# Kernel optimization log

Measured on AMD Instinct MI355X. Metric: run time of the kernel, lower is better.

Reference implementation:

```python
import jax, jax.numpy as jnp
import numpy as np


def _cell(xt, h, c, Wih, Whh, b):
    # Single LSTM cell step; PyTorch gate order i, f, g, o.
    g = xt @ Wih.T + h @ Whh.T + b
    i, f, gg, o = jnp.split(g, 4, axis=-1)
    c = jax.nn.sigmoid(f) * c + jax.nn.sigmoid(i) * jnp.tanh(gg)
    h = jax.nn.sigmoid(o) * jnp.tanh(c)
    return h, c


def _lstm_layer(x, Wih, Whh, b):
    # x: [B, T, D] -> hs: [B, T, H], (h, c): final states [B, H]
    B = x.shape[0]
    H = Whh.shape[1]
    h0 = jnp.zeros((B, H), x.dtype)
    c0 = jnp.zeros((B, H), x.dtype)

    def step(carry, xt):
        h, c = carry
        h, c = _cell(xt, h, c, Wih, Whh, b)
        return (h, c), h

    (h, c), hs = jax.lax.scan(step, (h0, c0), jnp.swapaxes(x, 0, 1))
    return jnp.swapaxes(hs, 0, 1), h, c


def setup_inputs() -> dict:
    key = jax.random.key(0)
    B, T_SRC, D_IN, H, TGT = 512, 256, 32, 128, 64
    ks = iter(jax.random.split(key, 32))
    s_in = 1.0 / np.sqrt(H)

    def u(k, shape):
        return jax.random.uniform(k, shape, jnp.float32, -s_in, s_in)

    inp = {"x": jax.random.normal(next(ks), (B, T_SRC, D_IN), jnp.float32),
           "target_len": TGT}
    for pre in ("enc", "dec"):
        for l, din in ((0, D_IN), (1, H)):
            inp[f"{pre}_Wih{l}"] = u(next(ks), (4 * H, din))
            inp[f"{pre}_Whh{l}"] = u(next(ks), (4 * H, H))
            inp[f"{pre}_bih{l}"] = u(next(ks), (4 * H,))
            inp[f"{pre}_bhh{l}"] = u(next(ks), (4 * H,))
    inp["lin_W"] = u(next(ks), (D_IN, H))
    inp["lin_b"] = u(next(ks), (D_IN,))
    return inp


def reference(x, target_len,
              enc_Wih0, enc_Whh0, enc_bih0, enc_bhh0,
              enc_Wih1, enc_Whh1, enc_bih1, enc_bhh1,
              dec_Wih0, dec_Whh0, dec_bih0, dec_bhh0,
              dec_Wih1, dec_Whh1, dec_bih1, dec_bhh1,
              lin_W, lin_b):
    # --- encoder: 2-layer full-sequence LSTM, zero initial state ---
    hs0, eh0, ec0 = _lstm_layer(x, enc_Wih0, enc_Whh0, enc_bih0 + enc_bhh0)
    _, eh1, ec1 = _lstm_layer(hs0, enc_Wih1, enc_Whh1, enc_bih1 + enc_bhh1)

    # --- decoder: recursive single-step LSTM + linear head, fed back ---
    db0 = dec_bih0 + dec_bhh0
    db1 = dec_bih1 + dec_bhh1
    dec_in0 = x[:, -1, :]  # last source step

    def step(carry, _):
        h0, c0, h1, c1, inp = carry
        h0, c0 = _cell(inp, h0, c0, dec_Wih0, dec_Whh0, db0)
        h1, c1 = _cell(h0, h1, c1, dec_Wih1, dec_Whh1, db1)
        out = h1 @ lin_W.T + lin_b
        return (h0, c0, h1, c1, out), out

    _, outs = jax.lax.scan(step, (eh0, ec0, eh1, ec1, dec_in0), None,
                           length=target_len)
    return jnp.swapaxes(outs, 0, 1)  # [B, target_len, input_size]
```

## Files before the change

### kernel.cpp

```cpp
#include <hip/hip_runtime.h>
#include <cstdint>
#include <cstddef>

typedef short  short8  __attribute__((ext_vector_type(8)));
typedef float  float4v __attribute__((ext_vector_type(4)));

#define MFMA_B16(a,b,c) __builtin_amdgcn_mfma_f32_16x16x32_bf16(a,b,c,0,0,0)

static constexpr int B_  = 512;
static constexpr int T_  = 256;
static constexpr int DIN = 32;
static constexpr int H_  = 128;
static constexpr int TGT = 64;

static constexpr float L2E  = 1.4426950408889634f;
static constexpr float L2E2 = 2.8853900817779268f;

static constexpr size_t OFF_XFRAG = 0;
static constexpr size_t OFF_EW0   = 8388608;
static constexpr size_t OFF_EW1LO = OFF_EW0   + 163840;
static constexpr size_t OFF_EW1HI = OFF_EW1LO + 131072;
static constexpr size_t OFF_DW0   = OFF_EW1HI + 131072;
static constexpr size_t OFF_DW1LO = OFF_DW0   + 163840;
static constexpr size_t OFF_DW1HI = OFF_DW1LO + 131072;
static constexpr size_t OFF_LIN   = OFF_DW1HI + 131072;
static constexpr size_t OFF_BIAS  = OFF_LIN   + 8192;
static constexpr size_t WS_NEED   = OFF_BIAS  + 8320;

static constexpr int SM_W    = 0;
static constexpr int SM_ABUF = 131072;
static constexpr int SM_INP  = 147712;
static constexpr int SM_LIN  = 148992;
static constexpr int SM_TOTAL= 157184;

__device__ __forceinline__ short f2bf(float f){
  unsigned u = __float_as_uint(f);
  unsigned r = (u + 0x7fffu + ((u>>16)&1u)) >> 16;
  return (short)(r & 0xffffu);
}
__device__ __forceinline__ float sigm2(float x){
  return __builtin_amdgcn_rcpf(1.f + __builtin_amdgcn_exp2f(-x));
}
__device__ __forceinline__ float st2(float a, float b){
  float ea = __builtin_amdgcn_exp2f(-a);
  float eb = __builtin_amdgcn_exp2f(-b);
  float d  = __builtin_amdgcn_rcpf((1.f+ea)*(1.f+eb));
  return (1.f-eb)*d;
}
__device__ __forceinline__ float st2c(float a, float c){
  float ea = __builtin_amdgcn_exp2f(-a);
  float eb = __builtin_amdgcn_exp2f(-L2E2*c);
  float d  = __builtin_amdgcn_rcpf((1.f+ea)*(1.f+eb));
  return (1.f-eb)*d;
}
__device__ __forceinline__ float gate_scale(int n){
  return ((n >> 7) == 2) ? L2E2 : L2E;
}

__global__ void prep_x_kernel(const float* __restrict__ x, short8* __restrict__ xfrag){
  int i = blockIdx.x*256 + threadIdx.x;
  if (i >= 32*256*64) return;
  int l    = i & 63;
  int t    = (i >> 6) & 255;
  int bblk = i >> 14;
  int b    = bblk*16 + (l & 15);
  const float* src = x + ((size_t)(b*T_ + t))*DIN + ((l>>4)*8);
  short8 v;
  #pragma unroll
  for (int j=0;j<8;j++) v[j] = f2bf(src[j]);
  xfrag[i] = v;
}

__device__ __forceinline__ void pack160(short8* __restrict__ dst,
                                        const float* __restrict__ Wih,
                                        const float* __restrict__ Whh,
                                        int e){
  int nt = e/320; int r = e%320; int kb = r/64; int l = r%64;
  int n  = nt*16 + (l&15);
  float s = gate_scale(n);
  short8 v;
  #pragma unroll
  for (int j=0;j<8;j++){
    int k = kb*32 + (l>>4)*8 + j;
    float f = (k < 32) ? Wih[n*32 + k] : Whh[n*128 + (k-32)];
    v[j] = f2bf(f*s);
  }
  dst[e] = v;
}
__device__ __forceinline__ void pack256s(short8* __restrict__ dlo, short8* __restrict__ dhi,
                                         const float* __restrict__ Wih,
                                         const float* __restrict__ Whh,
                                         int e){
  int nt = e/512; int r = e%512; int kb = r/64; int l = r%64;
  int n  = nt*16 + (l&15);
  float s = gate_scale(n);
  short8 v;
  #pragma unroll
  for (int j=0;j<8;j++){
    int k = kb*32 + (l>>4)*8 + j;
    float f = (k < 128) ? Wih[n*128 + k] : Whh[n*128 + (k-128)];
    v[j] = f2bf(f*s);
  }
  if (kb < 4) dlo[(nt*4 + kb)*64 + l]     = v;
  else        dhi[(nt*4 + (kb-4))*64 + l] = v;
}

__global__ void prep_w_kernel(
    const float* __restrict__ eWih0, const float* __restrict__ eWhh0,
    const float* __restrict__ eWih1, const float* __restrict__ eWhh1,
    const float* __restrict__ dWih0, const float* __restrict__ dWhh0,
    const float* __restrict__ dWih1, const float* __restrict__ dWhh1,
    const float* __restrict__ linW,
    const float* __restrict__ eb0a, const float* __restrict__ eb0b,
    const float* __restrict__ eb1a, const float* __restrict__ eb1b,
    const float* __restrict__ db0a, const float* __restrict__ db0b,
    const float* __restrict__ db1a, const float* __restrict__ db1b,
    const float* __restrict__ linb,
    short8* __restrict__ encW0,
    short8* __restrict__ encW1lo, short8* __restrict__ encW1hi,
    short8* __restrict__ decW0,
    short8* __restrict__ decW1lo, short8* __restrict__ decW1hi,
    short8* __restrict__ linT,  float* __restrict__ biases)
{
  int i = blockIdx.x*256 + threadIdx.x;
  if (i < 10240)       { pack160(encW0, eWih0, eWhh0, i); }
  else if (i < 26624)  { pack256s(encW1lo, encW1hi, eWih1, eWhh1, i-10240); }
  else if (i < 36864)  { pack160(decW0, dWih0, dWhh0, i-26624); }
  else if (i < 53248)  { pack256s(decW1lo, decW1hi, dWih1, dWhh1, i-36864); }
  else if (i < 53760)  {
    int e = i - 53248;
    int nt = e/256; int r = e%256; int kb = r/64; int l = r%64;
    int n = nt*16 + (l&15);
    short8 v;
    #pragma unroll
    for (int j=0;j<8;j++){
      int k = kb*32 + (l>>4)*8 + j;
      v[j] = f2bf(linW[n*128 + k]);
    }
    linT[e] = v;
  }
  else if (i < 55840)  {
    int e = i - 53760;
    float v;
    if      (e < 512)  v = (eb0a[e]       + eb0b[e]      ) * gate_scale(e);
    else if (e < 1024) v = (eb1a[e-512]   + eb1b[e-512]  ) * gate_scale(e-512);
    else if (e < 1536) v = (db0a[e-1024]  + db0b[e-1024] ) * gate_scale(e-1024);
    else if (e < 2048) v = (db1a[e-1536]  + db1b[e-1536] ) * gate_scale(e-1536);
    else               v = linb[e-2048];
    biases[e] = v;
  }
}

__global__ __launch_bounds__(512, 1) void lstm_main_kernel(
    const short8* __restrict__ xfrag,
    const short8* __restrict__ encW0,
    const short8* __restrict__ encW1lo, const short8* __restrict__ encW1hi,
    const short8* __restrict__ decW0,
    const short8* __restrict__ decW1lo, const short8* __restrict__ decW1hi,
    const short8* __restrict__ linT,  const float* __restrict__ biases,
    float* __restrict__ out)
{
  extern __shared__ __align__(16) char smem[];
  short8* Wlds        = (short8*)(smem + SM_W);
  short (*Abuf)[520]  = (short(*)[520])(smem + SM_ABUF);
  short (*inpA)[40]   = (short(*)[40])(smem + SM_INP);
  short8* Wlin        = (short8*)(smem + SM_LIN);

  const int tid  = threadIdx.x;
  const int w    = tid >> 6;
  const int l    = tid & 63;
  const int col  = l & 15;
  const int lq   = l >> 4;
  const int bblk = blockIdx.x;

  for (int i = tid; i < 8192; i += 512) Wlds[i] = encW1hi[i];
  for (int i = tid; i < 16*520; i += 512) ((short*)Abuf)[i] = 0;

  short8 W0r[4][5];
  short8 W1lo[4][4];
  #pragma unroll
  for (int i=0;i<4;i++){
    #pragma unroll
    for (int kb=0;kb<5;kb++) W0r[i][kb]  = encW0  [(size_t)(8*i+w)*320 + (size_t)kb*64 + l];
    #pragma unroll
    for (int kb=0;kb<4;kb++) W1lo[i][kb] = encW1lo[(size_t)(8*i+w)*256 + (size_t)kb*64 + l];
  }
  float bs0[4], bs1[4];
  #pragma unroll
  for (int i=0;i<4;i++){
    bs0[i] = biases[       (8*i+w)*16 + col];
    bs1[i] = biases[512 +  (8*i+w)*16 + col];
  }

  float c0[4] = {0.f,0.f,0.f,0.f};
  float c1[4] = {0.f,0.f,0.f,0.f};

  const short8* xf = xfrag + (size_t)bblk*T_*64 + l;
  short8 a0 = xf[0];
  __syncthreads();


  {
    short8 hp[4];
    #pragma unroll
    for (int kb=0;kb<4;kb++) hp[kb] = *(const short8*)&Abuf[col][128 + kb*32 + lq*8];
    float4v acc0[4];
    #pragma unroll
    for (int i4=0;i4<4;i4++){
      float4v a = {bs0[i4],bs0[i4],bs0[i4],bs0[i4]};
      a = MFMA_B16(a0, W0r[i4][0], a);
      #pragma unroll
      for (int kb=0;kb<4;kb++) a = MFMA_B16(hp[kb], W0r[i4][kb+1], a);
      acc0[i4] = a;
    }
    a0 = xf[64];
    #pragma unroll
    for (int q=0;q<4;q++){
      float cc = st2(acc0[0][q], acc0[2][q]);
      c0[q] = cc;
      Abuf[lq*4+q][0 + 16*w + col] = f2bf(st2c(acc0[3][q], cc));
    }
    __syncthreads();
  }

  #pragma unroll 2
  for (int i = 1; i < T_; i++){
    const int p_h0_r = ((i-1)&1)*128;
    const int p_h0_w = (i&1)*128;
    const int p_h1_r = 256 + (i&1)*128;
    const int p_h1_w = 256 + ((i-1)&1)*128;

    short8 hp[4], h1p[4];
    #pragma unroll
    for (int kb=0;kb<4;kb++) hp[kb]  = *(const short8*)&Abuf[col][p_h0_r + kb*32 + lq*8];
    #pragma unroll
    for (int kb=0;kb<4;kb++) h1p[kb] = *(const short8*)&Abuf[col][p_h1_r + kb*32 + lq*8];

    float4v acc0[4], acc1[4];
    #pragma unroll
    for (int i4=0;i4<4;i4++){
      float4v a = {bs0[i4],bs0[i4],bs0[i4],bs0[i4]};
      a = MFMA_B16(a0, W0r[i4][0], a);
      #pragma unroll
      for (int kb=0;kb<4;kb++) a = MFMA_B16(hp[kb], W0r[i4][kb+1], a);
      acc0[i4] = a;

      float4v b = {bs1[i4],bs1[i4],bs1[i4],bs1[i4]};
      #pragma unroll
      for (int kb=0;kb<4;kb++) b = MFMA_B16(hp[kb], W1lo[i4][kb], b);
      #pragma unroll
      for (int kb=0;kb<4;kb++){
        short8 wv = Wlds[((8*i4+w)*4 + kb)*64 + l];
        b = MFMA_B16(h1p[kb], wv, b);
      }
      acc1[i4] = b;
    }
    a0 = xf[(size_t)((i+1 < T_) ? i+1 : i)*64];

    #pragma unroll
    for (int q=0;q<4;q++){
      float cc = sigm2(acc0[1][q])*c0[q] + st2(acc0[0][q], acc0[2][q]);
      c0[q] = cc;
      Abuf[lq*4+q][p_h0_w + 16*w + col] = f2bf(st2c(acc0[3][q], cc));
    }
    #pragma unroll
    for (int q=0;q<4;q++){
      float cc = sigm2(acc1[1][q])*c1[q] + st2(acc1[0][q], acc1[2][q]);
      c1[q] = cc;
      Abuf[lq*4+q][p_h1_w + 16*w + col] = f2bf(st2c(acc1[3][q], cc));
    }
    __syncthreads();
  }

  {
    const int p_h0_r = 128;
    const int p_h1_r = 256 + 0;
    const int p_h1_w = 256 + 128;
    short8 hp[4], h1p[4];
    #pragma unroll
    for (int kb=0;kb<4;kb++) hp[kb]  = *(const short8*)&Abuf[col][p_h0_r + kb*32 + lq*8];
    #pragma unroll
    for (int kb=0;kb<4;kb++) h1p[kb] = *(const short8*)&Abuf[col][p_h1_r + kb*32 + lq*8];
    float4v acc1[4];
    #pragma unroll
    for (int i4=0;i4<4;i4++){
      float4v b = {bs1[i4],bs1[i4],bs1[i4],bs1[i4]};
      #pragma unroll
      for (int kb=0;kb<4;kb++) b = MFMA_B16(hp[kb], W1lo[i4][kb], b);
      #pragma unroll
      for (int kb=0;kb<4;kb++){
        short8 wv = Wlds[((8*i4+w)*4 + kb)*64 + l];
        b = MFMA_B16(h1p[kb], wv, b);
      }
      acc1[i4] = b;
    }
    #pragma unroll
    for (int q=0;q<4;q++){
      float cc = sigm2(acc1[1][q])*c1[q] + st2(acc1[0][q], acc1[2][q]);
      c1[q] = cc;
      Abuf[lq*4+q][p_h1_w + 16*w + col] = f2bf(st2c(acc1[3][q], cc));
    }
    __syncthreads();
  }

  for (int i = tid; i < 8192; i += 512) Wlds[i] = decW1hi[i];
  if (tid < 512) Wlin[tid] = linT[tid];
  #pragma unroll
  for (int i=0;i<4;i++){
    #pragma unroll
    for (int kb=0;kb<5;kb++) W0r[i][kb]  = decW0  [(size_t)(8*i+w)*320 + (size_t)kb*64 + l];
    #pragma unroll
    for (int kb=0;kb<4;kb++) W1lo[i][kb] = decW1lo[(size_t)(8*i+w)*256 + (size_t)kb*64 + l];
    bs0[i] = biases[1024 + (8*i+w)*16 + col];
    bs1[i] = biases[1536 + (8*i+w)*16 + col];
  }
  float blin = (w < 2) ? biases[2048 + w*16 + col] : 0.f;
  if (w == 0){
    *(short8*)&inpA[col][lq*8] = xf[(size_t)(T_-1)*64];
  }
  __syncthreads();

  #pragma unroll 2
  for (int td = 0; td < TGT; td++){
    const int h0r = ((td+1)&1) * 128;
    const int h0w = 128 - h0r;
    const int h1r = 256 + h0r;
    const int h1w = 256 + h0w;

    short8 a0d = *(const short8*)&inpA[col][lq*8];
    short8 ah[4];
    #pragma unroll
    for (int kb=0;kb<4;kb++) ah[kb] = *(const short8*)&Abuf[col][h0r + kb*32 + lq*8];
    float4v acc0[4];
    #pragma unroll
    for (int i=0;i<4;i++){
      float4v a = {bs0[i],bs0[i],bs0[i],bs0[i]};
      a = MFMA_B16(a0d, W0r[i][0], a);
      #pragma unroll
      for (int kb=0;kb<4;kb++) a = MFMA_B16(ah[kb], W0r[i][kb+1], a);
      acc0[i] = a;
    }
    #pragma unroll
    for (int q=0;q<4;q++){
      float cc = sigm2(acc0[1][q])*c0[q] + st2(acc0[0][q], acc0[2][q]);
      c0[q] = cc;
      Abuf[lq*4+q][h0w + 16*w + col] = f2bf(st2c(acc0[3][q], cc));
    }
    __syncthreads();

    short8 a1lo[4], a1hi[4];
    #pragma unroll
    for (int kb=0;kb<4;kb++) a1lo[kb] = *(const short8*)&Abuf[col][h0w + kb*32 + lq*8];
    #pragma unroll
    for (int kb=0;kb<4;kb++) a1hi[kb] = *(const short8*)&Abuf[col][h1r + kb*32 + lq*8];
    float4v acc1[4];
    #pragma unroll
    for (int i=0;i<4;i++){
      float4v a = {bs1[i],bs1[i],bs1[i],bs1[i]};
      #pragma unroll
      for (int kb=0;kb<4;kb++) a = MFMA_B16(a1lo[kb], W1lo[i][kb], a);
      #pragma unroll
      for (int kb=0;kb<4;kb++){
        short8 wv = Wlds[((8*i+w)*4 + kb)*64 + l];
        a = MFMA_B16(a1hi[kb], wv, a);
      }
      acc1[i] = a;
    }
    #pragma unroll
    for (int q=0;q<4;q++){
      float cc = sigm2(acc1[1][q])*c1[q] + st2(acc1[0][q], acc1[2][q]);
      c1[q] = cc;
      Abuf[lq*4+q][h1w + 16*w + col] = f2bf(st2c(acc1[3][q], cc));
    }
    __syncthreads();

    if (w < 2){
      short8 hf[4];
      #pragma unroll
      for (int kb=0;kb<4;kb++) hf[kb] = *(const short8*)&Abuf[col][h1w + kb*32 + lq*8];
      float4v a = {blin,blin,blin,blin};
      #pragma unroll
      for (int kb=0;kb<4;kb++){
        short8 wv = Wlin[(w*4+kb)*64 + l];
        a = MFMA_B16(hf[kb], wv, a);
      }
      #pragma unroll
      for (int q=0;q<4;q++){
        float v = a[q];
        int b = bblk*16 + lq*4 + q;
        out[((size_t)b*TGT + td)*DIN + (w*16 + col)] = v;
        inpA[lq*4+q][w*16 + col] = f2bf(v);
      }
    }
    __syncthreads();
  }
}

extern "C" void kernel_launch(void* const* d_in, const int* in_sizes, int n_in,
                              void* d_out, int out_size, void* d_ws, size_t ws_size,
                              hipStream_t stream) {
  const float* x      = (const float*)d_in[0];
  const float* eWih0  = (const float*)d_in[2];
  const float* eWhh0  = (const float*)d_in[3];
  const float* eb0a   = (const float*)d_in[4];
  const float* eb0b   = (const float*)d_in[5];
  const float* eWih1  = (const float*)d_in[6];
  const float* eWhh1  = (const float*)d_in[7];
  const float* eb1a   = (const float*)d_in[8];
  const float* eb1b   = (const float*)d_in[9];
  const float* dWih0  = (const float*)d_in[10];
  const float* dWhh0  = (const float*)d_in[11];
  const float* db0a   = (const float*)d_in[12];
  const float* db0b   = (const float*)d_in[13];
  const float* dWih1  = (const float*)d_in[14];
  const float* dWhh1  = (const float*)d_in[15];
  const float* db1a   = (const float*)d_in[16];
  const float* db1b   = (const float*)d_in[17];
  const float* linW   = (const float*)d_in[18];
  const float* linb   = (const float*)d_in[19];

  char* ws = (char*)d_ws;
  short8* xfrag   = (short8*)(ws + OFF_XFRAG);
  short8* encW0   = (short8*)(ws + OFF_EW0);
  short8* encW1lo = (short8*)(ws + OFF_EW1LO);
  short8* encW1hi = (short8*)(ws + OFF_EW1HI);
  short8* decW0   = (short8*)(ws + OFF_DW0);
  short8* decW1lo = (short8*)(ws + OFF_DW1LO);
  short8* decW1hi = (short8*)(ws + OFF_DW1HI);
  short8* linT    = (short8*)(ws + OFF_LIN);
  float*  biases  = (float*)(ws + OFF_BIAS);

  hipFuncSetAttribute((const void*)lstm_main_kernel,
                      hipFuncAttributeMaxDynamicSharedMemorySize, SM_TOTAL);

  prep_x_kernel<<<2048, 256, 0, stream>>>(x, xfrag);
  prep_w_kernel<<<219, 256, 0, stream>>>(
      eWih0,eWhh0,eWih1,eWhh1,dWih0,dWhh0,dWih1,dWhh1,linW,
      eb0a,eb0b,eb1a,eb1b,db0a,db0b,db1a,db1b,linb,
      encW0,encW1lo,encW1hi,decW0,decW1lo,decW1hi,linT,biases);
  lstm_main_kernel<<<32, 512, SM_TOTAL, stream>>>(
      xfrag, encW0, encW1lo, encW1hi, decW0, decW1lo, decW1hi,
      linT, biases, (float*)d_out);
}
```

Measured before the change: 683.2 us.

## Split layer-1 recurrent weights between LDS and per-step global loads; merge cell-state math

The layer-1 hidden-to-hidden weight block is split in two. One half stays in LDS and the other half is reloaded from global memory (L2-resident) into registers at every timestep, with an asm barrier so the compiler cannot hoist the loads. This halves LDS read traffic per step and shrinks the shared-memory footprint, at the cost of a global load per step on the serial recurrence. Separately, the cell-state update is rewritten to combine the forget, input and candidate terms over a single reciprocal, saving one rcp per element.

```diff
diff --git a/kernel.cpp b/kernel.cpp
--- a/kernel.cpp
+++ b/kernel.cpp
@@ -16,36 +16,38 @@
 static constexpr float L2E  = 1.4426950408889634f;
 static constexpr float L2E2 = 2.8853900817779268f;
 
-static constexpr size_t OFF_XFRAG = 0;
-static constexpr size_t OFF_EW0   = 8388608;
-static constexpr size_t OFF_EW1LO = OFF_EW0   + 163840;
-static constexpr size_t OFF_EW1HI = OFF_EW1LO + 131072;
-static constexpr size_t OFF_DW0   = OFF_EW1HI + 131072;
-static constexpr size_t OFF_DW1LO = OFF_DW0   + 163840;
-static constexpr size_t OFF_DW1HI = OFF_DW1LO + 131072;
-static constexpr size_t OFF_LIN   = OFF_DW1HI + 131072;
-static constexpr size_t OFF_BIAS  = OFF_LIN   + 8192;
-static constexpr size_t WS_NEED   = OFF_BIAS  + 8320;
+static constexpr size_t OFF_XFRAG  = 0;
+static constexpr size_t OFF_EW0    = 8388608;
+static constexpr size_t OFF_EW1LO  = OFF_EW0    + 163840;
+static constexpr size_t OFF_EW1MID = OFF_EW1LO  + 131072;
+static constexpr size_t OFF_EW1HI2 = OFF_EW1MID + 65536;
+static constexpr size_t OFF_DW0    = OFF_EW1HI2 + 65536;
+static constexpr size_t OFF_DW1LO  = OFF_DW0    + 163840;
+static constexpr size_t OFF_DW1MID = OFF_DW1LO  + 131072;
+static constexpr size_t OFF_DW1HI2 = OFF_DW1MID + 65536;
+static constexpr size_t OFF_LIN    = OFF_DW1HI2 + 65536;
+static constexpr size_t OFF_BIAS   = OFF_LIN    + 8192;
+static constexpr size_t WS_NEED    = OFF_BIAS   + 8320;
 
 static constexpr int SM_W    = 0;
-static constexpr int SM_ABUF = 131072;
-static constexpr int SM_INP  = 147712;
-static constexpr int SM_LIN  = 148992;
-static constexpr int SM_TOTAL= 157184;
+static constexpr int SM_ABUF = 65536;
+static constexpr int SM_INP  = 82176;
+static constexpr int SM_LIN  = 83456;
+static constexpr int SM_TOTAL= 91648;
 
 __device__ __forceinline__ short f2bf(float f){
   unsigned u = __float_as_uint(f);
   unsigned r = (u + 0x7fffu + ((u>>16)&1u)) >> 16;
   return (short)(r & 0xffffu);
 }
-__device__ __forceinline__ float sigm2(float x){
-  return __builtin_amdgcn_rcpf(1.f + __builtin_amdgcn_exp2f(-x));
-}
-__device__ __forceinline__ float st2(float a, float b){
-  float ea = __builtin_amdgcn_exp2f(-a);
-  float eb = __builtin_amdgcn_exp2f(-b);
-  float d  = __builtin_amdgcn_rcpf((1.f+ea)*(1.f+eb));
-  return (1.f-eb)*d;
+__device__ __forceinline__ float cell_c(float gi, float gf, float gg, float c){
+  float ei = __builtin_amdgcn_exp2f(-gi);
+  float ef = __builtin_amdgcn_exp2f(-gf);
+  float eg = __builtin_amdgcn_exp2f(-gg);
+  float P  = (1.f+ei)*(1.f+eg);
+  float F  = 1.f+ef;
+  float num = c*P + (1.f-eg)*F;
+  return num * __builtin_amdgcn_rcpf(F*P);
 }
 __device__ __forceinline__ float st2c(float a, float c){
   float ea = __builtin_amdgcn_exp2f(-a);
@@ -87,7 +89,9 @@
   }
   dst[e] = v;
 }
-__device__ __forceinline__ void pack256s(short8* __restrict__ dlo, short8* __restrict__ dhi,
+__device__ __forceinline__ void pack256s(short8* __restrict__ dlo,
+                                         short8* __restrict__ dmid,
+                                         short8* __restrict__ dhi2,
                                          const float* __restrict__ Wih,
                                          const float* __restrict__ Whh,
                                          int e){
@@ -101,8 +105,9 @@
     float f = (k < 128) ? Wih[n*128 + k] : Whh[n*128 + (k-128)];
     v[j] = f2bf(f*s);
   }
-  if (kb < 4) dlo[(nt*4 + kb)*64 + l]     = v;
-  else        dhi[(nt*4 + (kb-4))*64 + l] = v;
+  if      (kb < 4) dlo [(nt*4 +  kb   )*64 + l] = v;
+  else if (kb < 6) dmid[(nt*2 + (kb-4))*64 + l] = v;
+  else             dhi2[(nt*2 + (kb-6))*64 + l] = v;
 }
 
 __global__ void prep_w_kernel(
@@ -117,16 +122,16 @@
     const float* __restrict__ db1a, const float* __restrict__ db1b,
     const float* __restrict__ linb,
     short8* __restrict__ encW0,
-    short8* __restrict__ encW1lo, short8* __restrict__ encW1hi,
+    short8* __restrict__ encW1lo, short8* __restrict__ encW1mid, short8* __restrict__ encW1hi2,
     short8* __restrict__ decW0,
-    short8* __restrict__ decW1lo, short8* __restrict__ decW1hi,
+    short8* __restrict__ decW1lo, short8* __restrict__ decW1mid, short8* __restrict__ decW1hi2,
     short8* __restrict__ linT,  float* __restrict__ biases)
 {
   int i = blockIdx.x*256 + threadIdx.x;
   if (i < 10240)       { pack160(encW0, eWih0, eWhh0, i); }
-  else if (i < 26624)  { pack256s(encW1lo, encW1hi, eWih1, eWhh1, i-10240); }
+  else if (i < 26624)  { pack256s(encW1lo, encW1mid, encW1hi2, eWih1, eWhh1, i-10240); }
   else if (i < 36864)  { pack160(decW0, dWih0, dWhh0, i-26624); }
-  else if (i < 53248)  { pack256s(decW1lo, decW1hi, dWih1, dWhh1, i-36864); }
+  else if (i < 53248)  { pack256s(decW1lo, decW1mid, decW1hi2, dWih1, dWhh1, i-36864); }
   else if (i < 53760)  {
     int e = i - 53248;
     int nt = e/256; int r = e%256; int kb = r/64; int l = r%64;
@@ -154,9 +159,11 @@
 __global__ __launch_bounds__(512, 1) void lstm_main_kernel(
     const short8* __restrict__ xfrag,
     const short8* __restrict__ encW0,
-    const short8* __restrict__ encW1lo, const short8* __restrict__ encW1hi,
+    const short8* __restrict__ encW1lo, const short8* __restrict__ encW1mid,
+    const short8* __restrict__ encW1hi2,
     const short8* __restrict__ decW0,
-    const short8* __restrict__ decW1lo, const short8* __restrict__ decW1hi,
+    const short8* __restrict__ decW1lo, const short8* __restrict__ decW1mid,
+    const short8* __restrict__ decW1hi2,
     const short8* __restrict__ linT,  const float* __restrict__ biases,
     float* __restrict__ out)
 {
@@ -173,7 +180,7 @@
   const int lq   = l >> 4;
   const int bblk = blockIdx.x;
 
-  for (int i = tid; i < 8192; i += 512) Wlds[i] = encW1hi[i];
+  for (int i = tid; i < 4096; i += 512) Wlds[i] = encW1mid[i];
   for (int i = tid; i < 16*520; i += 512) ((short*)Abuf)[i] = 0;
 
   short8 W0r[4][5];
@@ -216,7 +223,7 @@
     a0 = xf[64];
     #pragma unroll
     for (int q=0;q<4;q++){
-      float cc = st2(acc0[0][q], acc0[2][q]);
+      float cc = cell_c(acc0[0][q], acc0[1][q], acc0[2][q], 0.f);
       c0[q] = cc;
       Abuf[lq*4+q][0 + 16*w + col] = f2bf(st2c(acc0[3][q], cc));
     }
@@ -230,6 +237,13 @@
     const int p_h1_r = 256 + (i&1)*128;
     const int p_h1_w = 256 + ((i-1)&1)*128;
 
+    const short8* gHi2 = encW1hi2;
+    asm volatile("" : "+v"(gHi2));
+    short8 wg[8];
+    #pragma unroll
+    for (int t8=0;t8<8;t8++)
+      wg[t8] = gHi2[(size_t)((8*(t8>>1)+w)*2 + (t8&1))*64 + l];
+
     short8 hp[4], h1p[4];
     #pragma unroll
     for (int kb=0;kb<4;kb++) hp[kb]  = *(const short8*)&Abuf[col][p_h0_r + kb*32 + lq*8];
@@ -248,24 +262,23 @@
       float4v b = {bs1[i4],bs1[i4],bs1[i4],bs1[i4]};
       #pragma unroll
       for (int kb=0;kb<4;kb++) b = MFMA_B16(hp[kb], W1lo[i4][kb], b);
-      #pragma unroll
-      for (int kb=0;kb<4;kb++){
-        short8 wv = Wlds[((8*i4+w)*4 + kb)*64 + l];
-        b = MFMA_B16(h1p[kb], wv, b);
-      }
+      b = MFMA_B16(h1p[0], Wlds[((8*i4+w)*2+0)*64 + l], b);
+      b = MFMA_B16(h1p[1], Wlds[((8*i4+w)*2+1)*64 + l], b);
+      b = MFMA_B16(h1p[2], wg[2*i4+0], b);
+      b = MFMA_B16(h1p[3], wg[2*i4+1], b);
       acc1[i4] = b;
     }
     a0 = xf[(size_t)((i+1 < T_) ? i+1 : i)*64];
 
     #pragma unroll
     for (int q=0;q<4;q++){
-      float cc = sigm2(acc0[1][q])*c0[q] + st2(acc0[0][q], acc0[2][q]);
+      float cc = cell_c(acc0[0][q], acc0[1][q], acc0[2][q], c0[q]);
       c0[q] = cc;
       Abuf[lq*4+q][p_h0_w + 16*w + col] = f2bf(st2c(acc0[3][q], cc));
     }
     #pragma unroll
     for (int q=0;q<4;q++){
-      float cc = sigm2(acc1[1][q])*c1[q] + st2(acc1[0][q], acc1[2][q]);
+      float cc = cell_c(acc1[0][q], acc1[1][q], acc1[2][q], c1[q]);
       c1[q] = cc;
       Abuf[lq*4+q][p_h1_w + 16*w + col] = f2bf(st2c(acc1[3][q], cc));
     }
@@ -276,6 +289,12 @@
     const int p_h0_r = 128;
     const int p_h1_r = 256 + 0;
     const int p_h1_w = 256 + 128;
+    const short8* gHi2 = encW1hi2;
+    asm volatile("" : "+v"(gHi2));
+    short8 wg[8];
+    #pragma unroll
+    for (int t8=0;t8<8;t8++)
+      wg[t8] = gHi2[(size_t)((8*(t8>>1)+w)*2 + (t8&1))*64 + l];
     short8 hp[4], h1p[4];
     #pragma unroll
     for (int kb=0;kb<4;kb++) hp[kb]  = *(const short8*)&Abuf[col][p_h0_r + kb*32 + lq*8];
@@ -287,23 +306,22 @@
       float4v b = {bs1[i4],bs1[i4],bs1[i4],bs1[i4]};
       #pragma unroll
       for (int kb=0;kb<4;kb++) b = MFMA_B16(hp[kb], W1lo[i4][kb], b);
-      #pragma unroll
-      for (int kb=0;kb<4;kb++){
-        short8 wv = Wlds[((8*i4+w)*4 + kb)*64 + l];
-        b = MFMA_B16(h1p[kb], wv, b);
-      }
+      b = MFMA_B16(h1p[0], Wlds[((8*i4+w)*2+0)*64 + l], b);
+      b = MFMA_B16(h1p[1], Wlds[((8*i4+w)*2+1)*64 + l], b);
+      b = MFMA_B16(h1p[2], wg[2*i4+0], b);
+      b = MFMA_B16(h1p[3], wg[2*i4+1], b);
       acc1[i4] = b;
     }
     #pragma unroll
     for (int q=0;q<4;q++){
-      float cc = sigm2(acc1[1][q])*c1[q] + st2(acc1[0][q], acc1[2][q]);
+      float cc = cell_c(acc1[0][q], acc1[1][q], acc1[2][q], c1[q]);
       c1[q] = cc;
       Abuf[lq*4+q][p_h1_w + 16*w + col] = f2bf(st2c(acc1[3][q], cc));
     }
     __syncthreads();
   }
 
-  for (int i = tid; i < 8192; i += 512) Wlds[i] = decW1hi[i];
+  for (int i = tid; i < 4096; i += 512) Wlds[i] = decW1mid[i];
   if (tid < 512) Wlin[tid] = linT[tid];
   #pragma unroll
   for (int i=0;i<4;i++){
@@ -342,12 +360,18 @@
     }
     #pragma unroll
     for (int q=0;q<4;q++){
-      float cc = sigm2(acc0[1][q])*c0[q] + st2(acc0[0][q], acc0[2][q]);
+      float cc = cell_c(acc0[0][q], acc0[1][q], acc0[2][q], c0[q]);
       c0[q] = cc;
       Abuf[lq*4+q][h0w + 16*w + col] = f2bf(st2c(acc0[3][q], cc));
     }
     __syncthreads();
 
+    const short8* gHi2 = decW1hi2;
+    asm volatile("" : "+v"(gHi2));
+    short8 wg[8];
+    #pragma unroll
+    for (int t8=0;t8<8;t8++)
+      wg[t8] = gHi2[(size_t)((8*(t8>>1)+w)*2 + (t8&1))*64 + l];
     short8 a1lo[4], a1hi[4];
     #pragma unroll
     for (int kb=0;kb<4;kb++) a1lo[kb] = *(const short8*)&Abuf[col][h0w + kb*32 + lq*8];
@@ -359,16 +383,15 @@
       float4v a = {bs1[i],bs1[i],bs1[i],bs1[i]};
       #pragma unroll
       for (int kb=0;kb<4;kb++) a = MFMA_B16(a1lo[kb], W1lo[i][kb], a);
-      #pragma unroll
-      for (int kb=0;kb<4;kb++){
-        short8 wv = Wlds[((8*i+w)*4 + kb)*64 + l];
-        a = MFMA_B16(a1hi[kb], wv, a);
-      }
+      a = MFMA_B16(a1hi[0], Wlds[((8*i+w)*2+0)*64 + l], a);
+      a = MFMA_B16(a1hi[1], Wlds[((8*i+w)*2+1)*64 + l], a);
+      a = MFMA_B16(a1hi[2], wg[2*i+0], a);
+      a = MFMA_B16(a1hi[3], wg[2*i+1], a);
       acc1[i] = a;
     }
     #pragma unroll
     for (int q=0;q<4;q++){
-      float cc = sigm2(acc1[1][q])*c1[q] + st2(acc1[0][q], acc1[2][q]);
+      float cc = cell_c(acc1[0][q], acc1[1][q], acc1[2][q], c1[q]);
       c1[q] = cc;
       Abuf[lq*4+q][h1w + 16*w + col] = f2bf(st2c(acc1[3][q], cc));
     }
@@ -420,15 +443,17 @@
   const float* linb   = (const float*)d_in[19];
 
   char* ws = (char*)d_ws;
-  short8* xfrag   = (short8*)(ws + OFF_XFRAG);
-  short8* encW0   = (short8*)(ws + OFF_EW0);
-  short8* encW1lo = (short8*)(ws + OFF_EW1LO);
-  short8* encW1hi = (short8*)(ws + OFF_EW1HI);
-  short8* decW0   = (short8*)(ws + OFF_DW0);
-  short8* decW1lo = (short8*)(ws + OFF_DW1LO);
-  short8* decW1hi = (short8*)(ws + OFF_DW1HI);
-  short8* linT    = (short8*)(ws + OFF_LIN);
-  float*  biases  = (float*)(ws + OFF_BIAS);
+  short8* xfrag    = (short8*)(ws + OFF_XFRAG);
+  short8* encW0    = (short8*)(ws + OFF_EW0);
+  short8* encW1lo  = (short8*)(ws + OFF_EW1LO);
+  short8* encW1mid = (short8*)(ws + OFF_EW1MID);
+  short8* encW1hi2 = (short8*)(ws + OFF_EW1HI2);
+  short8* decW0    = (short8*)(ws + OFF_DW0);
+  short8* decW1lo  = (short8*)(ws + OFF_DW1LO);
+  short8* decW1mid = (short8*)(ws + OFF_DW1MID);
+  short8* decW1hi2 = (short8*)(ws + OFF_DW1HI2);
+  short8* linT     = (short8*)(ws + OFF_LIN);
+  float*  biases   = (float*)(ws + OFF_BIAS);
 
   hipFuncSetAttribute((const void*)lstm_main_kernel,
                       hipFuncAttributeMaxDynamicSharedMemorySize, SM_TOTAL);
@@ -437,8 +462,10 @@
   prep_w_kernel<<<219, 256, 0, stream>>>(
       eWih0,eWhh0,eWih1,eWhh1,dWih0,dWhh0,dWih1,dWhh1,linW,
       eb0a,eb0b,eb1a,eb1b,db0a,db0b,db1a,db1b,linb,
-      encW0,encW1lo,encW1hi,decW0,decW1lo,decW1hi,linT,biases);
+      encW0,encW1lo,encW1mid,encW1hi2,decW0,decW1lo,decW1mid,decW1hi2,
+      linT,biases);
   lstm_main_kernel<<<32, 512, SM_TOTAL, stream>>>(
-      xfrag, encW0, encW1lo, encW1hi, decW0, decW1lo, decW1hi,
+      xfrag, encW0, encW1lo, encW1mid, encW1hi2,
+      decW0, decW1lo, decW1mid, decW1hi2,
       linT, biases, (float*)d_out);
 }
```

New measurement: 1.034 ms. 51.4% more time.

## Stream recurrent hi-half weights from global/L2 instead of LDS, fuse cell-state math

Applied to the files above, without the earlier changes.

The 128 KB LDS copy of the layer-1 recurrent weights and the linear head weights is removed. Each timestep now loads these operands straight from global memory, relying on L1/L2 caching, with an asm barrier so the compiler cannot hoist the loads. The cell-state update is also merged into one function that uses a single reciprocal instead of separate sigmoid and sigmoid*tanh reciprocals. This trades LDS traffic for global/L2 latency on every serial recurrent step, which could stall the latency-bound loop.

```diff
diff --git a/kernel.cpp b/kernel.cpp
--- a/kernel.cpp
+++ b/kernel.cpp
@@ -27,25 +27,19 @@
 static constexpr size_t OFF_BIAS  = OFF_LIN   + 8192;
 static constexpr size_t WS_NEED   = OFF_BIAS  + 8320;
 
-static constexpr int SM_W    = 0;
-static constexpr int SM_ABUF = 131072;
-static constexpr int SM_INP  = 147712;
-static constexpr int SM_LIN  = 148992;
-static constexpr int SM_TOTAL= 157184;
-
 __device__ __forceinline__ short f2bf(float f){
   unsigned u = __float_as_uint(f);
   unsigned r = (u + 0x7fffu + ((u>>16)&1u)) >> 16;
   return (short)(r & 0xffffu);
 }
-__device__ __forceinline__ float sigm2(float x){
-  return __builtin_amdgcn_rcpf(1.f + __builtin_amdgcn_exp2f(-x));
-}
-__device__ __forceinline__ float st2(float a, float b){
-  float ea = __builtin_amdgcn_exp2f(-a);
-  float eb = __builtin_amdgcn_exp2f(-b);
-  float d  = __builtin_amdgcn_rcpf((1.f+ea)*(1.f+eb));
-  return (1.f-eb)*d;
+__device__ __forceinline__ float cell_c(float gi, float gf, float gg, float c){
+  float ei = __builtin_amdgcn_exp2f(-gi);
+  float ef = __builtin_amdgcn_exp2f(-gf);
+  float eg = __builtin_amdgcn_exp2f(-gg);
+  float P  = (1.f+ei)*(1.f+eg);
+  float F  = 1.f+ef;
+  float num = c*P + (1.f-eg)*F;
+  return num * __builtin_amdgcn_rcpf(F*P);
 }
 __device__ __forceinline__ float st2c(float a, float c){
   float ea = __builtin_amdgcn_exp2f(-a);
@@ -160,11 +154,8 @@
     const short8* __restrict__ linT,  const float* __restrict__ biases,
     float* __restrict__ out)
 {
-  extern __shared__ __align__(16) char smem[];
-  short8* Wlds        = (short8*)(smem + SM_W);
-  short (*Abuf)[520]  = (short(*)[520])(smem + SM_ABUF);
-  short (*inpA)[40]   = (short(*)[40])(smem + SM_INP);
-  short8* Wlin        = (short8*)(smem + SM_LIN);
+  __shared__ __align__(16) short Abuf[16][520];
+  __shared__ __align__(16) short inpA[16][40];
 
   const int tid  = threadIdx.x;
   const int w    = tid >> 6;
@@ -173,7 +164,6 @@
   const int lq   = l >> 4;
   const int bblk = blockIdx.x;
 
-  for (int i = tid; i < 8192; i += 512) Wlds[i] = encW1hi[i];
   for (int i = tid; i < 16*520; i += 512) ((short*)Abuf)[i] = 0;
 
   short8 W0r[4][5];
@@ -216,7 +206,7 @@
     a0 = xf[64];
     #pragma unroll
     for (int q=0;q<4;q++){
-      float cc = st2(acc0[0][q], acc0[2][q]);
+      float cc = cell_c(acc0[0][q], acc0[1][q], acc0[2][q], 0.f);
       c0[q] = cc;
       Abuf[lq*4+q][0 + 16*w + col] = f2bf(st2c(acc0[3][q], cc));
     }
@@ -230,6 +220,9 @@
     const int p_h1_r = 256 + (i&1)*128;
     const int p_h1_w = 256 + ((i-1)&1)*128;
 
+    const short8* pHi = encW1hi;
+    asm volatile("" : "+v"(pHi));
+
     short8 hp[4], h1p[4];
     #pragma unroll
     for (int kb=0;kb<4;kb++) hp[kb]  = *(const short8*)&Abuf[col][p_h0_r + kb*32 + lq*8];
@@ -249,23 +242,21 @@
       #pragma unroll
       for (int kb=0;kb<4;kb++) b = MFMA_B16(hp[kb], W1lo[i4][kb], b);
       #pragma unroll
-      for (int kb=0;kb<4;kb++){
-        short8 wv = Wlds[((8*i4+w)*4 + kb)*64 + l];
-        b = MFMA_B16(h1p[kb], wv, b);
-      }
+      for (int kb=0;kb<4;kb++)
+        b = MFMA_B16(h1p[kb], pHi[(size_t)((8*i4+w)*4 + kb)*64 + l], b);
       acc1[i4] = b;
     }
     a0 = xf[(size_t)((i+1 < T_) ? i+1 : i)*64];
 
     #pragma unroll
     for (int q=0;q<4;q++){
-      float cc = sigm2(acc0[1][q])*c0[q] + st2(acc0[0][q], acc0[2][q]);
+      float cc = cell_c(acc0[0][q], acc0[1][q], acc0[2][q], c0[q]);
       c0[q] = cc;
       Abuf[lq*4+q][p_h0_w + 16*w + col] = f2bf(st2c(acc0[3][q], cc));
     }
     #pragma unroll
     for (int q=0;q<4;q++){
-      float cc = sigm2(acc1[1][q])*c1[q] + st2(acc1[0][q], acc1[2][q]);
+      float cc = cell_c(acc1[0][q], acc1[1][q], acc1[2][q], c1[q]);
       c1[q] = cc;
       Abuf[lq*4+q][p_h1_w + 16*w + col] = f2bf(st2c(acc1[3][q], cc));
     }
@@ -276,6 +267,8 @@
     const int p_h0_r = 128;
     const int p_h1_r = 256 + 0;
     const int p_h1_w = 256 + 128;
+    const short8* pHi = encW1hi;
+    asm volatile("" : "+v"(pHi));
     short8 hp[4], h1p[4];
     #pragma unroll
     for (int kb=0;kb<4;kb++) hp[kb]  = *(const short8*)&Abuf[col][p_h0_r + kb*32 + lq*8];
@@ -288,23 +281,19 @@
       #pragma unroll
       for (int kb=0;kb<4;kb++) b = MFMA_B16(hp[kb], W1lo[i4][kb], b);
       #pragma unroll
-      for (int kb=0;kb<4;kb++){
-        short8 wv = Wlds[((8*i4+w)*4 + kb)*64 + l];
-        b = MFMA_B16(h1p[kb], wv, b);
-      }
+      for (int kb=0;kb<4;kb++)
+        b = MFMA_B16(h1p[kb], pHi[(size_t)((8*i4+w)*4 + kb)*64 + l], b);
       acc1[i4] = b;
     }
     #pragma unroll
     for (int q=0;q<4;q++){
-      float cc = sigm2(acc1[1][q])*c1[q] + st2(acc1[0][q], acc1[2][q]);
+      float cc = cell_c(acc1[0][q], acc1[1][q], acc1[2][q], c1[q]);
       c1[q] = cc;
       Abuf[lq*4+q][p_h1_w + 16*w + col] = f2bf(st2c(acc1[3][q], cc));
     }
     __syncthreads();
   }
 
-  for (int i = tid; i < 8192; i += 512) Wlds[i] = decW1hi[i];
-  if (tid < 512) Wlin[tid] = linT[tid];
   #pragma unroll
   for (int i=0;i<4;i++){
     #pragma unroll
@@ -342,12 +331,14 @@
     }
     #pragma unroll
     for (int q=0;q<4;q++){
-      float cc = sigm2(acc0[1][q])*c0[q] + st2(acc0[0][q], acc0[2][q]);
+      float cc = cell_c(acc0[0][q], acc0[1][q], acc0[2][q], c0[q]);
       c0[q] = cc;
       Abuf[lq*4+q][h0w + 16*w + col] = f2bf(st2c(acc0[3][q], cc));
     }
     __syncthreads();
 
+    const short8* pHi = decW1hi;
+    asm volatile("" : "+v"(pHi));
     short8 a1lo[4], a1hi[4];
     #pragma unroll
     for (int kb=0;kb<4;kb++) a1lo[kb] = *(const short8*)&Abuf[col][h0w + kb*32 + lq*8];
@@ -360,15 +351,13 @@
       #pragma unroll
       for (int kb=0;kb<4;kb++) a = MFMA_B16(a1lo[kb], W1lo[i][kb], a);
       #pragma unroll
-      for (int kb=0;kb<4;kb++){
-        short8 wv = Wlds[((8*i+w)*4 + kb)*64 + l];
-        a = MFMA_B16(a1hi[kb], wv, a);
-      }
+      for (int kb=0;kb<4;kb++)
+        a = MFMA_B16(a1hi[kb], pHi[(size_t)((8*i+w)*4 + kb)*64 + l], a);
       acc1[i] = a;
     }
     #pragma unroll
     for (int q=0;q<4;q++){
-      float cc = sigm2(acc1[1][q])*c1[q] + st2(acc1[0][q], acc1[2][q]);
+      float cc = cell_c(acc1[0][q], acc1[1][q], acc1[2][q], c1[q]);
       c1[q] = cc;
       Abuf[lq*4+q][h1w + 16*w + col] = f2bf(st2c(acc1[3][q], cc));
     }
@@ -380,10 +369,8 @@
       for (int kb=0;kb<4;kb++) hf[kb] = *(const short8*)&Abuf[col][h1w + kb*32 + lq*8];
       float4v a = {blin,blin,blin,blin};
       #pragma unroll
-      for (int kb=0;kb<4;kb++){
-        short8 wv = Wlin[(w*4+kb)*64 + l];
-        a = MFMA_B16(hf[kb], wv, a);
-      }
+      for (int kb=0;kb<4;kb++)
+        a = MFMA_B16(hf[kb], linT[(size_t)(w*4+kb)*64 + l], a);
       #pragma unroll
       for (int q=0;q<4;q++){
         float v = a[q];
@@ -430,15 +417,12 @@
   short8* linT    = (short8*)(ws + OFF_LIN);
   float*  biases  = (float*)(ws + OFF_BIAS);
 
-  hipFuncSetAttribute((const void*)lstm_main_kernel,
-                      hipFuncAttributeMaxDynamicSharedMemorySize, SM_TOTAL);
-
   prep_x_kernel<<<2048, 256, 0, stream>>>(x, xfrag);
   prep_w_kernel<<<219, 256, 0, stream>>>(
       eWih0,eWhh0,eWih1,eWhh1,dWih0,dWhh0,dWih1,dWhh1,linW,
       eb0a,eb0b,eb1a,eb1b,db0a,db0b,db1a,db1b,linb,
       encW0,encW1lo,encW1hi,decW0,decW1lo,decW1hi,linT,biases);
-  lstm_main_kernel<<<32, 512, SM_TOTAL, stream>>>(
+  lstm_main_kernel<<<32, 512, 0, stream>>>(
       xfrag, encW0, encW1lo, encW1hi, decW0, decW1lo, decW1hi,
       linT, biases, (float*)d_out);
 }
```

Result: slower. 1.338 ms (+95.8%).

## Split LSTM layers across separate wave groups in a 1024-thread block

Applied to the files above, without the earlier changes.

The block grows from 512 to 1024 threads. Waves 0-7 compute layer 0 and waves 8-15 compute layer 1, where before each wave did both layers serially. Each step's two layer matmuls and gate math can therefore run concurrently on different waves, which shortens the serial chain per step. The gate math is also fused into one cell_c helper that uses a single reciprocal for the cell-state update. The trade-off is twice as many waves competing for the CU's MFMA units, more LDS traffic, and a lower register budget per thread.

```diff
diff --git a/kernel.cpp b/kernel.cpp
--- a/kernel.cpp
+++ b/kernel.cpp
@@ -38,14 +38,14 @@
   unsigned r = (u + 0x7fffu + ((u>>16)&1u)) >> 16;
   return (short)(r & 0xffffu);
 }
-__device__ __forceinline__ float sigm2(float x){
-  return __builtin_amdgcn_rcpf(1.f + __builtin_amdgcn_exp2f(-x));
-}
-__device__ __forceinline__ float st2(float a, float b){
-  float ea = __builtin_amdgcn_exp2f(-a);
-  float eb = __builtin_amdgcn_exp2f(-b);
-  float d  = __builtin_amdgcn_rcpf((1.f+ea)*(1.f+eb));
-  return (1.f-eb)*d;
+__device__ __forceinline__ float cell_c(float gi, float gf, float gg, float c){
+  float ei = __builtin_amdgcn_exp2f(-gi);
+  float ef = __builtin_amdgcn_exp2f(-gf);
+  float eg = __builtin_amdgcn_exp2f(-gg);
+  float P  = (1.f+ei)*(1.f+eg);
+  float F  = 1.f+ef;
+  float num = c*P + (1.f-eg)*F;
+  return num * __builtin_amdgcn_rcpf(F*P);
 }
 __device__ __forceinline__ float st2c(float a, float c){
   float ea = __builtin_amdgcn_exp2f(-a);
@@ -151,7 +151,7 @@
   }
 }
 
-__global__ __launch_bounds__(512, 1) void lstm_main_kernel(
+__global__ __launch_bounds__(1024, 1) void lstm_main_kernel(
     const short8* __restrict__ xfrag,
     const short8* __restrict__ encW0,
     const short8* __restrict__ encW1lo, const short8* __restrict__ encW1hi,
@@ -168,153 +168,112 @@
 
   const int tid  = threadIdx.x;
   const int w    = tid >> 6;
+  const int wl   = w & 7;
+  const bool isL0 = (w < 8);
   const int l    = tid & 63;
   const int col  = l & 15;
   const int lq   = l >> 4;
   const int bblk = blockIdx.x;
 
-  for (int i = tid; i < 8192; i += 512) Wlds[i] = encW1hi[i];
-  for (int i = tid; i < 16*520; i += 512) ((short*)Abuf)[i] = 0;
-
-  short8 W0r[4][5];
-  short8 W1lo[4][4];
+  for (int i = tid; i < 8192; i += 1024) Wlds[i] = encW1hi[i];
+  for (int i = tid; i < 16*520; i += 1024) ((short*)Abuf)[i] = 0;
+
+  short8 Wr[4][5];
+  float  bs[4];
   #pragma unroll
   for (int i=0;i<4;i++){
-    #pragma unroll
-    for (int kb=0;kb<5;kb++) W0r[i][kb]  = encW0  [(size_t)(8*i+w)*320 + (size_t)kb*64 + l];
-    #pragma unroll
-    for (int kb=0;kb<4;kb++) W1lo[i][kb] = encW1lo[(size_t)(8*i+w)*256 + (size_t)kb*64 + l];
-  }
-  float bs0[4], bs1[4];
-  #pragma unroll
-  for (int i=0;i<4;i++){
-    bs0[i] = biases[       (8*i+w)*16 + col];
-    bs1[i] = biases[512 +  (8*i+w)*16 + col];
-  }
-
-  float c0[4] = {0.f,0.f,0.f,0.f};
-  float c1[4] = {0.f,0.f,0.f,0.f};
+    int nt = 8*i + wl;
+    if (isL0){
+      #pragma unroll
+      for (int kb=0;kb<5;kb++) Wr[i][kb] = encW0[(size_t)nt*320 + (size_t)kb*64 + l];
+      bs[i] = biases[nt*16 + col];
+    } else {
+      #pragma unroll
+      for (int kb=0;kb<4;kb++) Wr[i][kb] = encW1lo[(size_t)nt*256 + (size_t)kb*64 + l];
+      bs[i] = biases[512 + nt*16 + col];
+    }
+  }
+
+  float cst[4] = {0.f,0.f,0.f,0.f};
 
   const short8* xf = xfrag + (size_t)bblk*T_*64 + l;
-  short8 a0 = xf[0];
+  short8 a0 = isL0 ? xf[0] : short8{};
   __syncthreads();
 
-
-  {
-    short8 hp[4];
-    #pragma unroll
-    for (int kb=0;kb<4;kb++) hp[kb] = *(const short8*)&Abuf[col][128 + kb*32 + lq*8];
-    float4v acc0[4];
-    #pragma unroll
-    for (int i4=0;i4<4;i4++){
-      float4v a = {bs0[i4],bs0[i4],bs0[i4],bs0[i4]};
-      a = MFMA_B16(a0, W0r[i4][0], a);
-      #pragma unroll
-      for (int kb=0;kb<4;kb++) a = MFMA_B16(hp[kb], W0r[i4][kb+1], a);
-      acc0[i4] = a;
-    }
-    a0 = xf[64];
-    #pragma unroll
-    for (int q=0;q<4;q++){
-      float cc = st2(acc0[0][q], acc0[2][q]);
-      c0[q] = cc;
-      Abuf[lq*4+q][0 + 16*w + col] = f2bf(st2c(acc0[3][q], cc));
+  #pragma unroll 2
+  for (int i = 0; i <= T_; i++){
+    const int p_h0_r = ((i-1)&1)*128;
+    if (isL0){
+      if (i < T_){
+        short8 hp[4];
+        #pragma unroll
+        for (int kb=0;kb<4;kb++) hp[kb] = *(const short8*)&Abuf[col][p_h0_r + kb*32 + lq*8];
+        float4v acc[4];
+        #pragma unroll
+        for (int i4=0;i4<4;i4++){
+          float4v a = {bs[i4],bs[i4],bs[i4],bs[i4]};
+          a = MFMA_B16(a0, Wr[i4][0], a);
+          #pragma unroll
+          for (int kb=0;kb<4;kb++) a = MFMA_B16(hp[kb], Wr[i4][kb+1], a);
+          acc[i4] = a;
+        }
+        a0 = xf[(size_t)((i+1 < T_) ? i+1 : i)*64];
+        #pragma unroll
+        for (int q=0;q<4;q++){
+          float cc = cell_c(acc[0][q], acc[1][q], acc[2][q], cst[q]);
+          cst[q] = cc;
+          Abuf[lq*4+q][(i&1)*128 + 16*wl + col] = f2bf(st2c(acc[3][q], cc));
+        }
+      }
+    } else {
+      if (i >= 1){
+        const int p_h1_r = 256 + (i&1)*128;
+        const int p_h1_w = 256 + ((i-1)&1)*128;
+        short8 hp[4], h1p[4];
+        #pragma unroll
+        for (int kb=0;kb<4;kb++) hp[kb]  = *(const short8*)&Abuf[col][p_h0_r + kb*32 + lq*8];
+        #pragma unroll
+        for (int kb=0;kb<4;kb++) h1p[kb] = *(const short8*)&Abuf[col][p_h1_r + kb*32 + lq*8];
+        float4v acc[4];
+        #pragma unroll
+        for (int i4=0;i4<4;i4++){
+          float4v b = {bs[i4],bs[i4],bs[i4],bs[i4]};
+          #pragma unroll
+          for (int kb=0;kb<4;kb++) b = MFMA_B16(hp[kb], Wr[i4][kb], b);
+          #pragma unroll
+          for (int kb=0;kb<4;kb++){
+            short8 wv = Wlds[((8*i4+wl)*4 + kb)*64 + l];
+            b = MFMA_B16(h1p[kb], wv, b);
+          }
+          acc[i4] = b;
+        }
+        #pragma unroll
+        for (int q=0;q<4;q++){
+          float cc = cell_c(acc[0][q], acc[1][q], acc[2][q], cst[q]);
+          cst[q] = cc;
+          Abuf[lq*4+q][p_h1_w + 16*wl + col] = f2bf(st2c(acc[3][q], cc));
+        }
+      }
     }
     __syncthreads();
   }
 
-  #pragma unroll 2
-  for (int i = 1; i < T_; i++){
-    const int p_h0_r = ((i-1)&1)*128;
-    const int p_h0_w = (i&1)*128;
-    const int p_h1_r = 256 + (i&1)*128;
-    const int p_h1_w = 256 + ((i-1)&1)*128;
-
-    short8 hp[4], h1p[4];
-    #pragma unroll
-    for (int kb=0;kb<4;kb++) hp[kb]  = *(const short8*)&Abuf[col][p_h0_r + kb*32 + lq*8];
-    #pragma unroll
-    for (int kb=0;kb<4;kb++) h1p[kb] = *(const short8*)&Abuf[col][p_h1_r + kb*32 + lq*8];
-
-    float4v acc0[4], acc1[4];
-    #pragma unroll
-    for (int i4=0;i4<4;i4++){
-      float4v a = {bs0[i4],bs0[i4],bs0[i4],bs0[i4]};
-      a = MFMA_B16(a0, W0r[i4][0], a);
-      #pragma unroll
-      for (int kb=0;kb<4;kb++) a = MFMA_B16(hp[kb], W0r[i4][kb+1], a);
-      acc0[i4] = a;
-
-      float4v b = {bs1[i4],bs1[i4],bs1[i4],bs1[i4]};
-      #pragma unroll
-      for (int kb=0;kb<4;kb++) b = MFMA_B16(hp[kb], W1lo[i4][kb], b);
-      #pragma unroll
-      for (int kb=0;kb<4;kb++){
-        short8 wv = Wlds[((8*i4+w)*4 + kb)*64 + l];
-        b = MFMA_B16(h1p[kb], wv, b);
-      }
-      acc1[i4] = b;
-    }
-    a0 = xf[(size_t)((i+1 < T_) ? i+1 : i)*64];
-
-    #pragma unroll
-    for (int q=0;q<4;q++){
-      float cc = sigm2(acc0[1][q])*c0[q] + st2(acc0[0][q], acc0[2][q]);
-      c0[q] = cc;
-      Abuf[lq*4+q][p_h0_w + 16*w + col] = f2bf(st2c(acc0[3][q], cc));
-    }
-    #pragma unroll
-    for (int q=0;q<4;q++){
-      float cc = sigm2(acc1[1][q])*c1[q] + st2(acc1[0][q], acc1[2][q]);
-      c1[q] = cc;
-      Abuf[lq*4+q][p_h1_w + 16*w + col] = f2bf(st2c(acc1[3][q], cc));
-    }
-    __syncthreads();
-  }
-
-  {
-    const int p_h0_r = 128;
-    const int p_h1_r = 256 + 0;
-    const int p_h1_w = 256 + 128;
-    short8 hp[4], h1p[4];
-    #pragma unroll
-    for (int kb=0;kb<4;kb++) hp[kb]  = *(const short8*)&Abuf[col][p_h0_r + kb*32 + lq*8];
-    #pragma unroll
-    for (int kb=0;kb<4;kb++) h1p[kb] = *(const short8*)&Abuf[col][p_h1_r + kb*32 + lq*8];
-    float4v acc1[4];
-    #pragma unroll
-    for (int i4=0;i4<4;i4++){
-      float4v b = {bs1[i4],bs1[i4],bs1[i4],bs1[i4]};
-      #pragma unroll
-      for (int kb=0;kb<4;kb++) b = MFMA_B16(hp[kb], W1lo[i4][kb], b);
-      #pragma unroll
-      for (int kb=0;kb<4;kb++){
-        short8 wv = Wlds[((8*i4+w)*4 + kb)*64 + l];
-        b = MFMA_B16(h1p[kb], wv, b);
-      }
-      acc1[i4] = b;
-    }
-    #pragma unroll
-    for (int q=0;q<4;q++){
-      float cc = sigm2(acc1[1][q])*c1[q] + st2(acc1[0][q], acc1[2][q]);
-      c1[q] = cc;
-      Abuf[lq*4+q][p_h1_w + 16*w + col] = f2bf(st2c(acc1[3][q], cc));
-    }
-    __syncthreads();
-  }
-
-  for (int i = tid; i < 8192; i += 512) Wlds[i] = decW1hi[i];
+  for (int i = tid; i < 8192; i += 1024) Wlds[i] = decW1hi[i];
   if (tid < 512) Wlin[tid] = linT[tid];
   #pragma unroll
   for (int i=0;i<4;i++){
-    #pragma unroll
-    for (int kb=0;kb<5;kb++) W0r[i][kb]  = decW0  [(size_t)(8*i+w)*320 + (size_t)kb*64 + l];
-    #pragma unroll
-    for (int kb=0;kb<4;kb++) W1lo[i][kb] = decW1lo[(size_t)(8*i+w)*256 + (size_t)kb*64 + l];
-    bs0[i] = biases[1024 + (8*i+w)*16 + col];
-    bs1[i] = biases[1536 + (8*i+w)*16 + col];
-  }
-  float blin = (w < 2) ? biases[2048 + w*16 + col] : 0.f;
+    int nt = 8*i + wl;
+    if (isL0){
+      #pragma unroll
+      for (int kb=0;kb<5;kb++) Wr[i][kb] = decW0[(size_t)nt*320 + (size_t)kb*64 + l];
+      bs[i] = biases[1024 + nt*16 + col];
+    } else {
+      #pragma unroll
+      for (int kb=0;kb<4;kb++) Wr[i][kb] = decW1lo[(size_t)nt*256 + (size_t)kb*64 + l];
+      bs[i] = biases[1536 + nt*16 + col];
+    }
+  }
+  float blin = (w >= 8 && w < 10) ? biases[2048 + (w-8)*16 + col] : 0.f;
   if (w == 0){
     *(short8*)&inpA[col][lq*8] = xf[(size_t)(T_-1)*64];
   }
@@ -327,69 +286,74 @@
     const int h1r = 256 + h0r;
     const int h1w = 256 + h0w;
 
-    short8 a0d = *(const short8*)&inpA[col][lq*8];
-    short8 ah[4];
-    #pragma unroll
-    for (int kb=0;kb<4;kb++) ah[kb] = *(const short8*)&Abuf[col][h0r + kb*32 + lq*8];
-    float4v acc0[4];
-    #pragma unroll
-    for (int i=0;i<4;i++){
-      float4v a = {bs0[i],bs0[i],bs0[i],bs0[i]};
-      a = MFMA_B16(a0d, W0r[i][0], a);
-      #pragma unroll
-      for (int kb=0;kb<4;kb++) a = MFMA_B16(ah[kb], W0r[i][kb+1], a);
-      acc0[i] = a;
-    }
-    #pragma unroll
-    for (int q=0;q<4;q++){
-      float cc = sigm2(acc0[1][q])*c0[q] + st2(acc0[0][q], acc0[2][q]);
-      c0[q] = cc;
-      Abuf[lq*4+q][h0w + 16*w + col] = f2bf(st2c(acc0[3][q], cc));
+    if (isL0){
+      short8 a0d = *(const short8*)&inpA[col][lq*8];
+      short8 ah[4];
+      #pragma unroll
+      for (int kb=0;kb<4;kb++) ah[kb] = *(const short8*)&Abuf[col][h0r + kb*32 + lq*8];
+      float4v acc[4];
+      #pragma unroll
+      for (int i=0;i<4;i++){
+        float4v a = {bs[i],bs[i],bs[i],bs[i]};
+        a = MFMA_B16(a0d, Wr[i][0], a);
+        #pragma unroll
+        for (int kb=0;kb<4;kb++) a = MFMA_B16(ah[kb], Wr[i][kb+1], a);
+        acc[i] = a;
+      }
+      #pragma unroll
+      for (int q=0;q<4;q++){
+        float cc = cell_c(acc[0][q], acc[1][q], acc[2][q], cst[q]);
+        cst[q] = cc;
+        Abuf[lq*4+q][h0w + 16*wl + col] = f2bf(st2c(acc[3][q], cc));
+      }
     }
     __syncthreads();
 
-    short8 a1lo[4], a1hi[4];
-    #pragma unroll
-    for (int kb=0;kb<4;kb++) a1lo[kb] = *(const short8*)&Abuf[col][h0w + kb*32 + lq*8];
-    #pragma unroll
-    for (int kb=0;kb<4;kb++) a1hi[kb] = *(const short8*)&Abuf[col][h1r + kb*32 + lq*8];
-    float4v acc1[4];
-    #pragma unroll
-    for (int i=0;i<4;i++){
-      float4v a = {bs1[i],bs1[i],bs1[i],bs1[i]};
-      #pragma unroll
-      for (int kb=0;kb<4;kb++) a = MFMA_B16(a1lo[kb], W1lo[i][kb], a);
-      #pragma unroll
-      for (int kb=0;kb<4;kb++){
-        short8 wv = Wlds[((8*i+w)*4 + kb)*64 + l];
-        a = MFMA_B16(a1hi[kb], wv, a);
-      }
-      acc1[i] = a;
-    }
-    #pragma unroll
-    for (int q=0;q<4;q++){
-      float cc = sigm2(acc1[1][q])*c1[q] + st2(acc1[0][q], acc1[2][q]);
-      c1[q] = cc;
-      Abuf[lq*4+q][h1w + 16*w + col] = f2bf(st2c(acc1[3][q], cc));
+    if (!isL0){
+      short8 a1lo[4], a1hi[4];
+      #pragma unroll
+      for (int kb=0;kb<4;kb++) a1lo[kb] = *(const short8*)&Abuf[col][h0w + kb*32 + lq*8];
+      #pragma unroll
+      for (int kb=0;kb<4;kb++) a1hi[kb] = *(const short8*)&Abuf[col][h1r + kb*32 + lq*8];
+      float4v acc[4];
+      #pragma unroll
+      for (int i=0;i<4;i++){
+        float4v a = {bs[i],bs[i],bs[i],bs[i]};
+        #pragma unroll
+        for (int kb=0;kb<4;kb++) a = MFMA_B16(a1lo[kb], Wr[i][kb], a);
+        #pragma unroll
+        for (int kb=0;kb<4;kb++){
+          short8 wv = Wlds[((8*i+wl)*4 + kb)*64 + l];
+          a = MFMA_B16(a1hi[kb], wv, a);
+        }
+        acc[i] = a;
+      }
+      #pragma unroll
+      for (int q=0;q<4;q++){
+        float cc = cell_c(acc[0][q], acc[1][q], acc[2][q], cst[q]);
+        cst[q] = cc;
+        Abuf[lq*4+q][h1w + 16*wl + col] = f2bf(st2c(acc[3][q], cc));
+      }
     }
     __syncthreads();
 
-    if (w < 2){
+    if (w >= 8 && w < 10){
+      const int wp = w - 8;
       short8 hf[4];
       #pragma unroll
       for (int kb=0;kb<4;kb++) hf[kb] = *(const short8*)&Abuf[col][h1w + kb*32 + lq*8];
       float4v a = {blin,blin,blin,blin};
       #pragma unroll
       for (int kb=0;kb<4;kb++){
-        short8 wv = Wlin[(w*4+kb)*64 + l];
+        short8 wv = Wlin[(wp*4+kb)*64 + l];
         a = MFMA_B16(hf[kb], wv, a);
       }
       #pragma unroll
       for (int q=0;q<4;q++){
         float v = a[q];
         int b = bblk*16 + lq*4 + q;
-        out[((size_t)b*TGT + td)*DIN + (w*16 + col)] = v;
-        inpA[lq*4+q][w*16 + col] = f2bf(v);
+        out[((size_t)b*TGT + td)*DIN + (wp*16 + col)] = v;
+        inpA[lq*4+q][wp*16 + col] = f2bf(v);
       }
     }
     __syncthreads();
@@ -438,7 +402,7 @@
       eWih0,eWhh0,eWih1,eWhh1,dWih0,dWhh0,dWih1,dWhh1,linW,
       eb0a,eb0b,eb1a,eb1b,db0a,db0b,db1a,db1b,linb,
       encW0,encW1lo,encW1hi,decW0,decW1lo,decW1hi,linT,biases);
-  lstm_main_kernel<<<32, 512, SM_TOTAL, stream>>>(
+  lstm_main_kernel<<<32, 1024, SM_TOTAL, stream>>>(
       xfrag, encW0, encW1lo, encW1hi, decW0, decW1lo, decW1hi,
       linT, biases, (float*)d_out);
 }
```

New measurement: 1.007 ms. 1.47x slower.
